# Kernel optimization log

Hardware: AMD Instinct MI355X
Metric: run time of the kernel (lower is better)

The kernel has to match this reference:

```python
import jax, jax.numpy as jnp
import numpy as np

HIDDEN = 1024
FEAT = 2048
BOTTLENECK = 512
B, T = 64, 512


def setup_inputs() -> dict:
    key = jax.random.key(0)
    k1, k2, k3, k4, k5 = jax.random.split(key, 5)
    hidden = jax.random.normal(k1, (B, HIDDEN), dtype=jnp.float32)
    feats = jax.random.normal(k2, (B, T, FEAT), dtype=jnp.float32)
    # nn.Linear weights stored as [out, in]; apply as x @ W.T
    W = jax.random.normal(k3, (BOTTLENECK, HIDDEN), dtype=jnp.float32) * (1.0 / np.sqrt(HIDDEN))
    U = jax.random.normal(k4, (BOTTLENECK, FEAT), dtype=jnp.float32) * (1.0 / np.sqrt(FEAT))
    b = jnp.ones((BOTTLENECK,), dtype=jnp.float32)
    w = jax.random.normal(k5, (1, BOTTLENECK), dtype=jnp.float32) * (1.0 / np.sqrt(BOTTLENECK))
    return {"hidden": hidden, "feats": feats, "W": W, "U": U, "b": b, "w": w}


def reference(hidden, feats, W, U, b, w):
    Wh = hidden @ W.T                      # [B, K]
    Uv = jnp.einsum('btf,kf->btk', feats, U)  # [B, T, K]
    e = jnp.tanh(Wh[:, None, :] + Uv + b)  # [B, T, K]
    energies = jnp.einsum('btk,ok->bto', e, w)  # [B, T, 1]
    weights = jax.nn.softmax(energies, axis=1)  # softmax over time
    attn_feats = jnp.sum(feats * weights, axis=1)  # [B, F]
    return attn_feats, weights
```

## Files before the change

kernel.cpp:

```cpp
#include <hip/hip_runtime.h>
#include <math.h>

#define BATCH 64
#define TDIM 512
#define FEAT 2048
#define HID 1024
#define KDIM 512
#define MROWS (BATCH * TDIM)
#define TCH 16
#define TCLEN (TDIM / TCH)

#define U4 (KDIM * FEAT / 4)

typedef __attribute__((ext_vector_type(8))) short short8;
typedef __attribute__((ext_vector_type(4))) float floatx4;

#define GLL16(g, l)                                                     \
    __builtin_amdgcn_global_load_lds(                                   \
        (const __attribute__((address_space(1))) void*)(g),             \
        (__attribute__((address_space(3))) void*)(l), 16, 0, 0)

__device__ __forceinline__ unsigned short f2bf(float x) {
    unsigned int u = __float_as_uint(x);
    u += 0x7FFFu + ((u >> 16) & 1u);
    return (unsigned short)(u >> 16);
}

__global__ __launch_bounds__(256) void k0n(const float* __restrict__ U,
                                           const float* __restrict__ hidden,
                                           const float* __restrict__ W,
                                           const float* __restrict__ bias,
                                           unsigned short* __restrict__ uB,
                                           float* __restrict__ whb) {
    int bx = blockIdx.x;
    if (bx < 256) {
        int stride = 256 * 256;
        for (int i = bx * 256 + threadIdx.x; i < U4; i += stride) {
            float4 v = ((const float4*)U)[i];
            ushort4 o;
            o.x = f2bf(v.x); o.y = f2bf(v.y); o.z = f2bf(v.z); o.w = f2bf(v.w);
            ((ushort4*)uB)[i] = o;
        }
    } else {
        int bid = bx - 256;
        int b = bid >> 7;
        int k = (bid & 127) * 4 + (threadIdx.x >> 6);
        int lane = threadIdx.x & 63;
        const float* hrow = hidden + (size_t)b * HID;
        const float* wrow = W + (size_t)k * HID;
        float acc = 0.f;
        #pragma unroll 4
        for (int h = lane; h < HID; h += 64) acc += hrow[h] * wrow[h];
        #pragma unroll
        for (int off = 32; off > 0; off >>= 1) acc += __shfl_down(acc, off, 64);
        if (lane == 0) whb[b * KDIM + k] = acc + bias[k];
    }
}

__global__ __launch_bounds__(512, 2) void k2n(const float* __restrict__ feats,
                                              const unsigned short* __restrict__ uB,
                                              const float* __restrict__ whb,
                                              const float* __restrict__ wvec,
                                              float* __restrict__ energies) {
    __shared__ __align__(16) unsigned short As[128 * 64];
    __shared__ __align__(16) unsigned short Bs[512 * 64];
    __shared__ float sums[4][128];

    const int tid  = threadIdx.x;
    const int wave = tid >> 6;
    const int lane = tid & 63;
    const int row0 = blockIdx.x * 128;
    const int wm = wave >> 2;
    const int wn = wave & 3;
    const int col = lane & 15, quad = lane >> 4;

    const int sr = tid >> 3;
    const int sc = (tid & 7) ^ (sr & 7);
    const float* gA = feats + (size_t)(row0 + sr) * FEAT + sc * 8;
    unsigned short* lA0 = As + tid * 8;
    unsigned short* lA1 = As + (tid + 512) * 8;

    const int bq = (lane & 7) ^ ((lane >> 3) & 7);
    const int br = wave * 8 + (lane >> 3);
    const unsigned short* gBp[8];
    unsigned short* lB[8];
    #pragma unroll
    for (int g = 0; g < 8; ++g) {
        gBp[g] = uB + (size_t)(g * 64 + br) * FEAT + bq * 8;
        lB[g]  = Bs + (g * 512 + wave * 64) * 8;
    }

    floatx4 acc[4][8];
    #pragma unroll
    for (int i = 0; i < 4; ++i)
        #pragma unroll
        for (int j = 0; j < 8; ++j) acc[i][j] = (floatx4){0.f, 0.f, 0.f, 0.f};

    float4 a0 = *(const float4*)(gA);
    float4 a1 = *(const float4*)(gA + 4);
    float4 a2 = *(const float4*)(gA + (size_t)64 * FEAT);
    float4 a3 = *(const float4*)(gA + (size_t)64 * FEAT + 4);
    gA += 64;

    for (int f0 = 0; f0 < FEAT; f0 += 64) {
        #pragma unroll
        for (int g = 0; g < 8; ++g) { GLL16(gBp[g], lB[g]); gBp[g] += 64; }
        short8 w0, w1;
        w0[0] = f2bf(a0.x); w0[1] = f2bf(a0.y); w0[2] = f2bf(a0.z); w0[3] = f2bf(a0.w);
        w0[4] = f2bf(a1.x); w0[5] = f2bf(a1.y); w0[6] = f2bf(a1.z); w0[7] = f2bf(a1.w);
        w1[0] = f2bf(a2.x); w1[1] = f2bf(a2.y); w1[2] = f2bf(a2.z); w1[3] = f2bf(a2.w);
        w1[4] = f2bf(a3.x); w1[5] = f2bf(a3.y); w1[6] = f2bf(a3.z); w1[7] = f2bf(a3.w);
        *(short8*)lA0 = w0;
        *(short8*)lA1 = w1;
        __syncthreads();

        if (f0 + 64 < FEAT) {
            a0 = *(const float4*)(gA);
            a1 = *(const float4*)(gA + 4);
            a2 = *(const float4*)(gA + (size_t)64 * FEAT);
            a3 = *(const float4*)(gA + (size_t)64 * FEAT + 4);
            gA += 64;
        }

        #pragma unroll
        for (int kk = 0; kk < 2; ++kk) {
            const int sw = ((kk * 4 + quad) ^ (col & 7)) * 8;
            short8 af[4], bf[8];
            #pragma unroll
            for (int i = 0; i < 4; ++i)
                af[i] = *(const short8*)&As[(wm * 64 + i * 16 + col) * 64 + sw];
            #pragma unroll
            for (int j = 0; j < 8; ++j)
                bf[j] = *(const short8*)&Bs[(wn * 128 + j * 16 + col) * 64 + sw];
            #pragma unroll
            for (int i = 0; i < 4; ++i)
                #pragma unroll
                for (int j = 0; j < 8; ++j)
                    acc[i][j] = __builtin_amdgcn_mfma_f32_16x16x32_bf16(
                        af[i], bf[j], acc[i][j], 0, 0, 0);
        }
        __syncthreads();
    }

    const int b = row0 >> 9;
    float wk[8], hk[8];
    #pragma unroll
    for (int j = 0; j < 8; ++j) {
        int k = wn * 128 + j * 16 + col;
        wk[j] = wvec[k];
        hk[j] = whb[b * KDIM + k];
    }
    #pragma unroll
    for (int i = 0; i < 4; ++i) {
        #pragma unroll
        for (int r = 0; r < 4; ++r) {
            float s = 0.f;
            #pragma unroll
            for (int j = 0; j < 8; ++j)
                s += tanhf(acc[i][j][r] + hk[j]) * wk[j];
            #pragma unroll
            for (int off = 8; off > 0; off >>= 1)
                s += __shfl_down(s, off, 16);
            if (col == 0)
                sums[wn][wm * 64 + i * 16 + quad * 4 + r] = s;
        }
    }
    __syncthreads();
    if (tid < 128)
        energies[row0 + tid] =
            sums[0][tid] + sums[1][tid] + sums[2][tid] + sums[3][tid];
}

__global__ __launch_bounds__(512) void k3n(const float* __restrict__ energies,
                                           float* __restrict__ wout) {
    int b = blockIdx.x;
    int t = threadIdx.x;
    float e = energies[b * TDIM + t];

    __shared__ float sm[512];
    sm[t] = e;
    __syncthreads();
    #pragma unroll
    for (int s = 256; s > 0; s >>= 1) {
        if (t < s) sm[t] = fmaxf(sm[t], sm[t + s]);
        __syncthreads();
    }
    float m = sm[0];
    __syncthreads();
    float ex = __expf(e - m);
    sm[t] = ex;
    __syncthreads();
    #pragma unroll
    for (int s = 256; s > 0; s >>= 1) {
        if (t < s) sm[t] += sm[t + s];
        __syncthreads();
    }
    float inv = 1.f / sm[0];
    wout[b * TDIM + t] = ex * inv;
}

__global__ __launch_bounds__(256) void k4n(const float* __restrict__ feats,
                                           const float* __restrict__ weights,
                                           float* __restrict__ partial4) {
    int b  = blockIdx.y;
    int t0 = blockIdx.x * TCLEN;
    int f8 = threadIdx.x * 8;
    __shared__ float wsm[TCLEN];
    if (threadIdx.x < TCLEN) wsm[threadIdx.x] = weights[b * TDIM + t0 + threadIdx.x];
    __syncthreads();

    const float* fp = feats + ((size_t)b * TDIM + t0) * FEAT + f8;
    float a[8];
    #pragma unroll
    for (int e = 0; e < 8; ++e) a[e] = 0.f;
    #pragma unroll 4
    for (int t = 0; t < TCLEN; ++t) {
        float4 v0 = *(const float4*)(fp + (size_t)t * FEAT);
        float4 v1 = *(const float4*)(fp + (size_t)t * FEAT + 4);
        float w = wsm[t];
        a[0] += v0.x * w; a[1] += v0.y * w; a[2] += v0.z * w; a[3] += v0.w * w;
        a[4] += v1.x * w; a[5] += v1.y * w; a[6] += v1.z * w; a[7] += v1.w * w;
    }
    float* op = partial4 + ((size_t)blockIdx.x * BATCH + b) * FEAT + f8;
    float4 o0 = {a[0], a[1], a[2], a[3]};
    float4 o1 = {a[4], a[5], a[6], a[7]};
    *(float4*)op = o0;
    *(float4*)(op + 4) = o1;
}

__global__ __launch_bounds__(256) void k5_reduce(const float* __restrict__ partial4,
                                                 float* __restrict__ out) {
    int i4 = blockIdx.x * 256 + threadIdx.x;
    float4 s = ((const float4*)partial4)[i4];
    #pragma unroll
    for (int c = 1; c < TCH; ++c) {
        float4 v = ((const float4*)partial4)[(size_t)c * (BATCH * FEAT / 4) + i4];
        s.x += v.x; s.y += v.y; s.z += v.z; s.w += v.w;
    }
    ((float4*)out)[i4] = s;
}

#define BM 128
#define BN 128
#define BF 16
#define LDSPAD 4

__global__ __launch_bounds__(256) void k1_whb(const float* __restrict__ hidden,
                                              const float* __restrict__ W,
                                              const float* __restrict__ bias,
                                              float* __restrict__ whb) {
    int b = blockIdx.y;
    int k = blockIdx.x * 4 + (threadIdx.x >> 6);
    int lane = threadIdx.x & 63;
    const float* hrow = hidden + (size_t)b * HID;
    const float* wrow = W + (size_t)k * HID;
    float acc = 0.f;
    #pragma unroll 4
    for (int h = lane; h < HID; h += 64) acc += hrow[h] * wrow[h];
    #pragma unroll
    for (int off = 32; off > 0; off >>= 1) acc += __shfl_down(acc, off, 64);
    if (lane == 0) whb[b * KDIM + k] = acc + bias[k];
}

__global__ __launch_bounds__(256) void k2_energy(const float* __restrict__ feats,
                                                 const float* __restrict__ U,
                                                 const float* __restrict__ whb,
                                                 const float* __restrict__ wvec,
                                                 float* __restrict__ partial) {
    __shared__ __align__(16) float As[BF][BM + LDSPAD];
    __shared__ __align__(16) float Us[BF][BN + LDSPAD];

    const int row0 = blockIdx.x * BM;
    const int k0   = blockIdx.y * BN;
    const int tid  = threadIdx.x;
    const int tx   = tid & 15;
    const int ty   = tid >> 4;

    float acc[8][8];
    #pragma unroll
    for (int i = 0; i < 8; ++i)
        #pragma unroll
        for (int j = 0; j < 8; ++j) acc[i][j] = 0.f;

    for (int f0 = 0; f0 < FEAT; f0 += BF) {
        #pragma unroll
        for (int l = 0; l < 2; ++l) {
            int li = tid + l * 256;
            int r  = li >> 2;
            int c4 = (li & 3) * 4;
            float4 av = *(const float4*)(feats + (size_t)(row0 + r) * FEAT + f0 + c4);
            float4 uv = *(const float4*)(U     + (size_t)(k0   + r) * FEAT + f0 + c4);
            As[c4 + 0][r] = av.x; As[c4 + 1][r] = av.y;
            As[c4 + 2][r] = av.z; As[c4 + 3][r] = av.w;
            Us[c4 + 0][r] = uv.x; Us[c4 + 1][r] = uv.y;
            Us[c4 + 2][r] = uv.z; Us[c4 + 3][r] = uv.w;
        }
        __syncthreads();
        #pragma unroll
        for (int kf = 0; kf < BF; ++kf) {
            float4 a0 = *(const float4*)&As[kf][ty * 8];
            float4 a1 = *(const float4*)&As[kf][ty * 8 + 4];
            float4 u0 = *(const float4*)&Us[kf][tx * 8];
            float4 u1 = *(const float4*)&Us[kf][tx * 8 + 4];
            float a[8] = {a0.x, a0.y, a0.z, a0.w, a1.x, a1.y, a1.z, a1.w};
            float u[8] = {u0.x, u0.y, u0.z, u0.w, u1.x, u1.y, u1.z, u1.w};
            #pragma unroll
            for (int i = 0; i < 8; ++i)
                #pragma unroll
                for (int j = 0; j < 8; ++j) acc[i][j] += a[i] * u[j];
        }
        __syncthreads();
    }

    const int b = row0 >> 9;
    float psum[8];
    #pragma unroll
    for (int i = 0; i < 8; ++i) {
        float s = 0.f;
        #pragma unroll
        for (int j = 0; j < 8; ++j) {
            int k = k0 + tx * 8 + j;
            s += tanhf(acc[i][j] + whb[b * KDIM + k]) * wvec[k];
        }
        psum[i] = s;
    }
    #pragma unroll
    for (int off = 8; off > 0; off >>= 1)
        #pragma unroll
        for (int i = 0; i < 8; ++i) psum[i] += __shfl_down(psum[i], off, 16);

    if (tx == 0) {
        int c = blockIdx.y;
        #pragma unroll
        for (int i = 0; i < 8; ++i)
            partial[c * MROWS + row0 + ty * 8 + i] = psum[i];
    }
}

__global__ __launch_bounds__(512) void k3_softmax(const float* __restrict__ partial,
                                                  float* __restrict__ wout) {
    int b = blockIdx.x;
    int t = threadIdx.x;
    float e = 0.f;
    #pragma unroll
    for (int c = 0; c < 4; ++c) e += partial[c * MROWS + b * TDIM + t];

    __shared__ float sm[512];
    sm[t] = e;
    __syncthreads();
    #pragma unroll
    for (int s = 256; s > 0; s >>= 1) {
        if (t < s) sm[t] = fmaxf(sm[t], sm[t + s]);
        __syncthreads();
    }
    float m = sm[0];
    __syncthreads();
    float ex = __expf(e - m);
    sm[t] = ex;
    __syncthreads();
    #pragma unroll
    for (int s = 256; s > 0; s >>= 1) {
        if (t < s) sm[t] += sm[t + s];
        __syncthreads();
    }
    float inv = 1.f / sm[0];
    wout[b * TDIM + t] = ex * inv;
}

__global__ __launch_bounds__(256) void k4_direct(const float* __restrict__ feats,
                                                 const float* __restrict__ weights,
                                                 float* __restrict__ out) {
    int b = blockIdx.y;
    int f4 = (blockIdx.x * 256 + threadIdx.x) * 4;
    __shared__ float wsm[TDIM];
    wsm[threadIdx.x]       = weights[b * TDIM + threadIdx.x];
    wsm[threadIdx.x + 256] = weights[b * TDIM + 256 + threadIdx.x];
    __syncthreads();

    const float* fp = feats + (size_t)b * TDIM * FEAT + f4;
    float ax = 0.f, ay = 0.f, az = 0.f, aw = 0.f;
    for (int t = 0; t < TDIM; ++t) {
        float4 v = *(const float4*)(fp + (size_t)t * FEAT);
        float w = wsm[t];
        ax += v.x * w; ay += v.y * w; az += v.z * w; aw += v.w * w;
    }
    float4 o = {ax, ay, az, aw};
    *(float4*)(out + (size_t)b * FEAT + f4) = o;
}

extern "C" void kernel_launch(void* const* d_in, const int* in_sizes, int n_in,
                              void* d_out, int out_size, void* d_ws, size_t ws_size,
                              hipStream_t stream) {
    const float* hidden = (const float*)d_in[0];
    const float* feats  = (const float*)d_in[1];
    const float* W      = (const float*)d_in[2];
    const float* U      = (const float*)d_in[3];
    const float* bias   = (const float*)d_in[4];
    const float* wvec   = (const float*)d_in[5];

    float* out         = (float*)d_out;
    float* attn_out    = out;
    float* weights_out = out + (size_t)BATCH * FEAT;
    float* whb         = weights_out;
    float* energies    = attn_out;

    const size_t uN        = (size_t)KDIM * FEAT;
    const size_t uBytes    = uN * sizeof(unsigned short);
    const size_t poolBytes = (size_t)TCH * BATCH * FEAT * sizeof(float);
    const bool fast = ws_size >= uBytes + poolBytes;

    if (fast) {
        unsigned short* uBf = (unsigned short*)d_ws;
        float* pool4 = (float*)((char*)d_ws + uBytes);
        k0n<<<dim3(256 + 8192), 256, 0, stream>>>(U, hidden, W, bias, uBf, whb);
        k2n<<<dim3(MROWS / 128), 512, 0, stream>>>(feats, uBf, whb, wvec, energies);
        k3n<<<dim3(BATCH), 512, 0, stream>>>(energies, weights_out);
        k4n<<<dim3(TCH, BATCH), 256, 0, stream>>>(feats, weights_out, pool4);
        k5_reduce<<<dim3(BATCH * FEAT / 4 / 256), 256, 0, stream>>>(pool4, attn_out);
    } else {
        k1_whb<<<dim3(KDIM / 4, BATCH), 256, 0, stream>>>(hidden, W, bias, whb);
        k2_energy<<<dim3(MROWS / 128, KDIM / 128), 256, 0, stream>>>(
            feats, U, whb, wvec, energies);
        k3_softmax<<<dim3(BATCH), 512, 0, stream>>>(energies, weights_out);
        k4_direct<<<dim3(FEAT / 1024, BATCH), 256, 0, stream>>>(
            feats, weights_out, attn_out);
    }
}
```

Before: 490.9 us.

## Pre-tile bf16 U into swizzled tiles and double-buffer B in LDS

The U-to-bf16 conversion now writes U already arranged in per-step, pre-swizzled 64-column tiles, so each wave's B loads come from one contiguous region. The energy GEMM kernel gets a second LDS buffer for B and issues the global-to-LDS copy for the next K step before running the MFMAs on the current one. The feats A tile is still single-buffered, with its conversion and store moved after the compute barrier. The aim is to hide B load latency behind the matrix math, at the cost of about 146KB of LDS per block and an extra barrier per step.

```diff
diff --git a/kernel.cpp b/kernel.cpp
--- a/kernel.cpp
+++ b/kernel.cpp
@@ -10,7 +10,9 @@
 #define TCH 16
 #define TCLEN (TDIM / TCH)
 
-#define U4 (KDIM * FEAT / 4)
+#define NSTEP (FEAT / 64)
+#define BSLOT (KDIM * 8)
+#define BTILE (BSLOT * 8)
 
 typedef __attribute__((ext_vector_type(8))) short short8;
 typedef __attribute__((ext_vector_type(4))) float floatx4;
@@ -30,16 +32,24 @@
                                            const float* __restrict__ hidden,
                                            const float* __restrict__ W,
                                            const float* __restrict__ bias,
-                                           unsigned short* __restrict__ uB,
+                                           unsigned short* __restrict__ uBt,
                                            float* __restrict__ whb) {
     int bx = blockIdx.x;
     if (bx < 256) {
-        int stride = 256 * 256;
-        for (int i = bx * 256 + threadIdx.x; i < U4; i += stride) {
-            float4 v = ((const float4*)U)[i];
-            ushort4 o;
-            o.x = f2bf(v.x); o.y = f2bf(v.y); o.z = f2bf(v.z); o.w = f2bf(v.w);
-            ((ushort4*)uB)[i] = o;
+        const int NS = NSTEP * BSLOT;
+        for (int s = bx * 256 + threadIdx.x; s < NS; s += 256 * 256) {
+            int t   = s >> 12;
+            int rem = s & 4095;
+            int r   = rem >> 3;
+            int c   = (rem & 7) ^ (r & 7);
+            const float* src = U + (size_t)r * FEAT + t * 64 + c * 8;
+            float4 v0 = *(const float4*)src;
+            float4 v1 = *(const float4*)(src + 4);
+            ushort4 o0, o1;
+            o0.x = f2bf(v0.x); o0.y = f2bf(v0.y); o0.z = f2bf(v0.z); o0.w = f2bf(v0.w);
+            o1.x = f2bf(v1.x); o1.y = f2bf(v1.y); o1.z = f2bf(v1.z); o1.w = f2bf(v1.w);
+            ((ushort4*)uBt)[s * 2]     = o0;
+            ((ushort4*)uBt)[s * 2 + 1] = o1;
         }
     } else {
         int bid = bx - 256;
@@ -58,12 +68,12 @@
 }
 
 __global__ __launch_bounds__(512, 2) void k2n(const float* __restrict__ feats,
-                                              const unsigned short* __restrict__ uB,
+                                              const unsigned short* __restrict__ uBt,
                                               const float* __restrict__ whb,
                                               const float* __restrict__ wvec,
                                               float* __restrict__ energies) {
     __shared__ __align__(16) unsigned short As[128 * 64];
-    __shared__ __align__(16) unsigned short Bs[512 * 64];
+    __shared__ __align__(16) unsigned short Bs[2][512 * 64];
     __shared__ float sums[4][128];
 
     const int tid  = threadIdx.x;
@@ -80,15 +90,7 @@
     unsigned short* lA0 = As + tid * 8;
     unsigned short* lA1 = As + (tid + 512) * 8;
 
-    const int bq = (lane & 7) ^ ((lane >> 3) & 7);
-    const int br = wave * 8 + (lane >> 3);
-    const unsigned short* gBp[8];
-    unsigned short* lB[8];
-    #pragma unroll
-    for (int g = 0; g < 8; ++g) {
-        gBp[g] = uB + (size_t)(g * 64 + br) * FEAT + bq * 8;
-        lB[g]  = Bs + (g * 512 + wave * 64) * 8;
-    }
+    const unsigned short* gB = uBt + (size_t)(wave * 512 + lane) * 8;
 
     floatx4 acc[4][8];
     #pragma unroll
@@ -101,10 +103,10 @@
     float4 a2 = *(const float4*)(gA + (size_t)64 * FEAT);
     float4 a3 = *(const float4*)(gA + (size_t)64 * FEAT + 4);
     gA += 64;
-
-    for (int f0 = 0; f0 < FEAT; f0 += 64) {
-        #pragma unroll
-        for (int g = 0; g < 8; ++g) { GLL16(gBp[g], lB[g]); gBp[g] += 64; }
+    #pragma unroll
+    for (int g = 0; g < 8; ++g)
+        GLL16(gB + g * 512, &Bs[0][(wave * 512 + g * 64) * 8]);
+    {
         short8 w0, w1;
         w0[0] = f2bf(a0.x); w0[1] = f2bf(a0.y); w0[2] = f2bf(a0.z); w0[3] = f2bf(a0.w);
         w0[4] = f2bf(a1.x); w0[5] = f2bf(a1.y); w0[6] = f2bf(a1.z); w0[7] = f2bf(a1.w);
@@ -112,14 +114,22 @@
         w1[4] = f2bf(a3.x); w1[5] = f2bf(a3.y); w1[6] = f2bf(a3.z); w1[7] = f2bf(a3.w);
         *(short8*)lA0 = w0;
         *(short8*)lA1 = w1;
-        __syncthreads();
-
-        if (f0 + 64 < FEAT) {
+    }
+    __syncthreads();
+
+    int nb = 0;
+    for (int t = 0; t < NSTEP; ++t) {
+        if (t < NSTEP - 1) {
             a0 = *(const float4*)(gA);
             a1 = *(const float4*)(gA + 4);
             a2 = *(const float4*)(gA + (size_t)64 * FEAT);
             a3 = *(const float4*)(gA + (size_t)64 * FEAT + 4);
             gA += 64;
+            const unsigned short* gb = gB + (size_t)(t + 1) * BTILE;
+            unsigned short* lb = &Bs[nb ^ 1][(wave * 512) * 8];
+            #pragma unroll
+            for (int g = 0; g < 8; ++g)
+                GLL16(gb + g * 512, lb + g * 512);
         }
 
         #pragma unroll
@@ -131,7 +141,7 @@
                 af[i] = *(const short8*)&As[(wm * 64 + i * 16 + col) * 64 + sw];
             #pragma unroll
             for (int j = 0; j < 8; ++j)
-                bf[j] = *(const short8*)&Bs[(wn * 128 + j * 16 + col) * 64 + sw];
+                bf[j] = *(const short8*)&Bs[nb][(wn * 128 + j * 16 + col) * 64 + sw];
             #pragma unroll
             for (int i = 0; i < 4; ++i)
                 #pragma unroll
@@ -140,6 +150,18 @@
                         af[i], bf[j], acc[i][j], 0, 0, 0);
         }
         __syncthreads();
+
+        if (t < NSTEP - 1) {
+            short8 w0, w1;
+            w0[0] = f2bf(a0.x); w0[1] = f2bf(a0.y); w0[2] = f2bf(a0.z); w0[3] = f2bf(a0.w);
+            w0[4] = f2bf(a1.x); w0[5] = f2bf(a1.y); w0[6] = f2bf(a1.z); w0[7] = f2bf(a1.w);
+            w1[0] = f2bf(a2.x); w1[1] = f2bf(a2.y); w1[2] = f2bf(a2.z); w1[3] = f2bf(a2.w);
+            w1[4] = f2bf(a3.x); w1[5] = f2bf(a3.y); w1[6] = f2bf(a3.z); w1[7] = f2bf(a3.w);
+            *(short8*)lA0 = w0;
+            *(short8*)lA1 = w1;
+            __syncthreads();
+        }
+        nb ^= 1;
     }
 
     const int b = row0 >> 9;
@@ -410,10 +432,10 @@
     const bool fast = ws_size >= uBytes + poolBytes;
 
     if (fast) {
-        unsigned short* uBf = (unsigned short*)d_ws;
+        unsigned short* uBt = (unsigned short*)d_ws;
         float* pool4 = (float*)((char*)d_ws + uBytes);
-        k0n<<<dim3(256 + 8192), 256, 0, stream>>>(U, hidden, W, bias, uBf, whb);
-        k2n<<<dim3(MROWS / 128), 512, 0, stream>>>(feats, uBf, whb, wvec, energies);
+        k0n<<<dim3(256 + 8192), 256, 0, stream>>>(U, hidden, W, bias, uBt, whb);
+        k2n<<<dim3(MROWS / 128), 512, 0, stream>>>(feats, uBt, whb, wvec, energies);
         k3n<<<dim3(BATCH), 512, 0, stream>>>(energies, weights_out);
         k4n<<<dim3(TCH, BATCH), 256, 0, stream>>>(feats, weights_out, pool4);
         k5_reduce<<<dim3(BATCH * FEAT / 4 / 256), 256, 0, stream>>>(pool4, attn_out);
```

After: 499.6 us. About the same (+1.8%).

## Fuse all stages into one persistent kernel with global barriers

Applied to the files above, without the earlier changes.

Replaces the five-kernel pipeline (U conversion plus Wh, energy GEMM, softmax, weighted sum, reduction) with one 256-block persistent kernel. The stages are separated by an atomic grid barrier. The time-axis split for the weighted sum drops from 16 chunks to 4, and each block recomputes its batch's softmax in shared memory. This removes kernel launch gaps and shrinks the partial-sum buffer. In exchange it relies on all blocks being co-resident, spins on global atomics, and runs the feature pass with fewer, longer-running blocks.

```diff
diff --git a/kernel.cpp b/kernel.cpp
--- a/kernel.cpp
+++ b/kernel.cpp
@@ -7,10 +7,6 @@
 #define HID 1024
 #define KDIM 512
 #define MROWS (BATCH * TDIM)
-#define TCH 16
-#define TCLEN (TDIM / TCH)
-
-#define U4 (KDIM * FEAT / 4)
 
 typedef __attribute__((ext_vector_type(8))) short short8;
 typedef __attribute__((ext_vector_type(4))) float floatx4;
@@ -26,218 +22,229 @@
     return (unsigned short)(u >> 16);
 }
 
-__global__ __launch_bounds__(256) void k0n(const float* __restrict__ U,
-                                           const float* __restrict__ hidden,
-                                           const float* __restrict__ W,
-                                           const float* __restrict__ bias,
-                                           unsigned short* __restrict__ uB,
-                                           float* __restrict__ whb) {
-    int bx = blockIdx.x;
-    if (bx < 256) {
-        int stride = 256 * 256;
-        for (int i = bx * 256 + threadIdx.x; i < U4; i += stride) {
-            float4 v = ((const float4*)U)[i];
-            ushort4 o;
-            o.x = f2bf(v.x); o.y = f2bf(v.y); o.z = f2bf(v.z); o.w = f2bf(v.w);
-            ((ushort4*)uB)[i] = o;
-        }
-    } else {
-        int bid = bx - 256;
-        int b = bid >> 7;
-        int k = (bid & 127) * 4 + (threadIdx.x >> 6);
-        int lane = threadIdx.x & 63;
-        const float* hrow = hidden + (size_t)b * HID;
-        const float* wrow = W + (size_t)k * HID;
-        float acc = 0.f;
-        #pragma unroll 4
-        for (int h = lane; h < HID; h += 64) acc += hrow[h] * wrow[h];
-        #pragma unroll
-        for (int off = 32; off > 0; off >>= 1) acc += __shfl_down(acc, off, 64);
-        if (lane == 0) whb[b * KDIM + k] = acc + bias[k];
-    }
-}
-
-__global__ __launch_bounds__(512, 2) void k2n(const float* __restrict__ feats,
-                                              const unsigned short* __restrict__ uB,
-                                              const float* __restrict__ whb,
-                                              const float* __restrict__ wvec,
-                                              float* __restrict__ energies) {
+__device__ __forceinline__ void gbar(unsigned* cnt, unsigned* gen, int nblk) {
+    __syncthreads();
+    __threadfence();
+    if (threadIdx.x == 0) {
+        unsigned g = __hip_atomic_load(gen, __ATOMIC_ACQUIRE,
+                                       __HIP_MEMORY_SCOPE_AGENT);
+        unsigned a = __hip_atomic_fetch_add(cnt, 1u, __ATOMIC_ACQ_REL,
+                                            __HIP_MEMORY_SCOPE_AGENT);
+        if (a == (unsigned)(nblk - 1)) {
+            __hip_atomic_store(cnt, 0u, __ATOMIC_RELAXED,
+                               __HIP_MEMORY_SCOPE_AGENT);
+            __hip_atomic_fetch_add(gen, 1u, __ATOMIC_RELEASE,
+                                   __HIP_MEMORY_SCOPE_AGENT);
+        } else {
+            long long t0 = (long long)clock64();
+            while (__hip_atomic_load(gen, __ATOMIC_ACQUIRE,
+                                     __HIP_MEMORY_SCOPE_AGENT) == g) {
+                __builtin_amdgcn_s_sleep(8);
+                if ((long long)clock64() - t0 > 100000000LL) break;
+            }
+        }
+    }
+    __syncthreads();
+    __threadfence();
+}
+
+__global__ __launch_bounds__(64) void k_init(unsigned* __restrict__ bar) {
+    if (threadIdx.x < 16) bar[threadIdx.x] = 0u;
+}
+
+__global__ __launch_bounds__(512) void mega(
+    const float* __restrict__ feats, const float* __restrict__ U,
+    const float* __restrict__ hidden, const float* __restrict__ W,
+    const float* __restrict__ bias, const float* __restrict__ wvec,
+    unsigned short* __restrict__ uB, float* __restrict__ pool4,
+    unsigned* __restrict__ bar,
+    float* __restrict__ whb, float* __restrict__ energies,
+    float* __restrict__ weights_out, float* __restrict__ attn_out) {
     __shared__ __align__(16) unsigned short As[128 * 64];
     __shared__ __align__(16) unsigned short Bs[512 * 64];
     __shared__ float sums[4][128];
+    __shared__ float sm[512];
 
     const int tid  = threadIdx.x;
+    const int bx   = blockIdx.x;
     const int wave = tid >> 6;
     const int lane = tid & 63;
-    const int row0 = blockIdx.x * 128;
-    const int wm = wave >> 2;
-    const int wn = wave & 3;
-    const int col = lane & 15, quad = lane >> 4;
-
-    const int sr = tid >> 3;
-    const int sc = (tid & 7) ^ (sr & 7);
-    const float* gA = feats + (size_t)(row0 + sr) * FEAT + sc * 8;
-    unsigned short* lA0 = As + tid * 8;
-    unsigned short* lA1 = As + (tid + 512) * 8;
-
-    const int bq = (lane & 7) ^ ((lane >> 3) & 7);
-    const int br = wave * 8 + (lane >> 3);
-    const unsigned short* gBp[8];
-    unsigned short* lB[8];
-    #pragma unroll
-    for (int g = 0; g < 8; ++g) {
-        gBp[g] = uB + (size_t)(g * 64 + br) * FEAT + bq * 8;
-        lB[g]  = Bs + (g * 512 + wave * 64) * 8;
-    }
-
-    floatx4 acc[4][8];
-    #pragma unroll
-    for (int i = 0; i < 4; ++i)
-        #pragma unroll
-        for (int j = 0; j < 8; ++j) acc[i][j] = (floatx4){0.f, 0.f, 0.f, 0.f};
-
-    float4 a0 = *(const float4*)(gA);
-    float4 a1 = *(const float4*)(gA + 4);
-    float4 a2 = *(const float4*)(gA + (size_t)64 * FEAT);
-    float4 a3 = *(const float4*)(gA + (size_t)64 * FEAT + 4);
-    gA += 64;
-
-    for (int f0 = 0; f0 < FEAT; f0 += 64) {
-        #pragma unroll
-        for (int g = 0; g < 8; ++g) { GLL16(gBp[g], lB[g]); gBp[g] += 64; }
-        short8 w0, w1;
-        w0[0] = f2bf(a0.x); w0[1] = f2bf(a0.y); w0[2] = f2bf(a0.z); w0[3] = f2bf(a0.w);
-        w0[4] = f2bf(a1.x); w0[5] = f2bf(a1.y); w0[6] = f2bf(a1.z); w0[7] = f2bf(a1.w);
-        w1[0] = f2bf(a2.x); w1[1] = f2bf(a2.y); w1[2] = f2bf(a2.z); w1[3] = f2bf(a2.w);
-        w1[4] = f2bf(a3.x); w1[5] = f2bf(a3.y); w1[6] = f2bf(a3.z); w1[7] = f2bf(a3.w);
-        *(short8*)lA0 = w0;
-        *(short8*)lA1 = w1;
-        __syncthreads();
-
-        if (f0 + 64 < FEAT) {
-            a0 = *(const float4*)(gA);
-            a1 = *(const float4*)(gA + 4);
-            a2 = *(const float4*)(gA + (size_t)64 * FEAT);
-            a3 = *(const float4*)(gA + (size_t)64 * FEAT + 4);
-            gA += 64;
-        }
-
-        #pragma unroll
-        for (int kk = 0; kk < 2; ++kk) {
-            const int sw = ((kk * 4 + quad) ^ (col & 7)) * 8;
-            short8 af[4], bf[8];
-            #pragma unroll
-            for (int i = 0; i < 4; ++i)
-                af[i] = *(const short8*)&As[(wm * 64 + i * 16 + col) * 64 + sw];
-            #pragma unroll
-            for (int j = 0; j < 8; ++j)
-                bf[j] = *(const short8*)&Bs[(wn * 128 + j * 16 + col) * 64 + sw];
-            #pragma unroll
-            for (int i = 0; i < 4; ++i)
+    unsigned* cnt = bar;
+    unsigned* gen = bar + 1;
+
+    {
+        const int i2 = (bx * 512 + tid) * 2;
+        #pragma unroll
+        for (int r = 0; r < 2; ++r) {
+            float4 v = ((const float4*)U)[i2 + r];
+            ushort4 o;
+            o.x = f2bf(v.x); o.y = f2bf(v.y); o.z = f2bf(v.z); o.w = f2bf(v.w);
+            ((ushort4*)uB)[i2 + r] = o;
+        }
+        const int gw = bx * 8 + wave;
+        for (int o = gw * 16; o < gw * 16 + 16; ++o) {
+            const int b = o >> 9, k = o & 511;
+            const float* hrow = hidden + (size_t)b * HID;
+            const float* wrow = W + (size_t)k * HID;
+            float acc = 0.f;
+            #pragma unroll 4
+            for (int h = lane; h < HID; h += 64) acc += hrow[h] * wrow[h];
+            #pragma unroll
+            for (int off = 32; off > 0; off >>= 1) acc += __shfl_down(acc, off, 64);
+            if (lane == 0) whb[o] = acc + bias[k];
+        }
+    }
+    gbar(cnt, gen, 256);
+
+    {
+        const int row0 = bx * 128;
+        const int wm = wave >> 2;
+        const int wn = wave & 3;
+        const int col = lane & 15, quad = lane >> 4;
+
+        const int sr = tid >> 3;
+        const int sc = (tid & 7) ^ (sr & 7);
+        const float* gA = feats + (size_t)(row0 + sr) * FEAT + sc * 8;
+        unsigned short* lA0 = As + tid * 8;
+        unsigned short* lA1 = As + (tid + 512) * 8;
+
+        const int bq = (lane & 7) ^ ((lane >> 3) & 7);
+        const int br = wave * 8 + (lane >> 3);
+        const unsigned short* gBp[8];
+        unsigned short* lB[8];
+        #pragma unroll
+        for (int g = 0; g < 8; ++g) {
+            gBp[g] = uB + (size_t)(g * 64 + br) * FEAT + bq * 8;
+            lB[g]  = Bs + (g * 512 + wave * 64) * 8;
+        }
+
+        floatx4 acc[4][8];
+        #pragma unroll
+        for (int i = 0; i < 4; ++i)
+            #pragma unroll
+            for (int j = 0; j < 8; ++j) acc[i][j] = (floatx4){0.f, 0.f, 0.f, 0.f};
+
+        float4 a0 = *(const float4*)(gA);
+        float4 a1 = *(const float4*)(gA + 4);
+        float4 a2 = *(const float4*)(gA + (size_t)64 * FEAT);
+        float4 a3 = *(const float4*)(gA + (size_t)64 * FEAT + 4);
+        gA += 64;
+
+        for (int f0 = 0; f0 < FEAT; f0 += 64) {
+            #pragma unroll
+            for (int g = 0; g < 8; ++g) { GLL16(gBp[g], lB[g]); gBp[g] += 64; }
+            short8 w0, w1;
+            w0[0] = f2bf(a0.x); w0[1] = f2bf(a0.y); w0[2] = f2bf(a0.z); w0[3] = f2bf(a0.w);
+            w0[4] = f2bf(a1.x); w0[5] = f2bf(a1.y); w0[6] = f2bf(a1.z); w0[7] = f2bf(a1.w);
+            w1[0] = f2bf(a2.x); w1[1] = f2bf(a2.y); w1[2] = f2bf(a2.z); w1[3] = f2bf(a2.w);
+            w1[4] = f2bf(a3.x); w1[5] = f2bf(a3.y); w1[6] = f2bf(a3.z); w1[7] = f2bf(a3.w);
+            *(short8*)lA0 = w0;
+            *(short8*)lA1 = w1;
+            __syncthreads();
+
+            if (f0 + 64 < FEAT) {
+                a0 = *(const float4*)(gA);
+                a1 = *(const float4*)(gA + 4);
+                a2 = *(const float4*)(gA + (size_t)64 * FEAT);
+                a3 = *(const float4*)(gA + (size_t)64 * FEAT + 4);
+                gA += 64;
+            }
+
+            #pragma unroll
+            for (int kk = 0; kk < 2; ++kk) {
+                const int sw = ((kk * 4 + quad) ^ (col & 7)) * 8;
+                short8 af[4], bf[8];
+                #pragma unroll
+                for (int i = 0; i < 4; ++i)
+                    af[i] = *(const short8*)&As[(wm * 64 + i * 16 + col) * 64 + sw];
                 #pragma unroll
                 for (int j = 0; j < 8; ++j)
-                    acc[i][j] = __builtin_amdgcn_mfma_f32_16x16x32_bf16(
-                        af[i], bf[j], acc[i][j], 0, 0, 0);
-        }
-        __syncthreads();
-    }
-
-    const int b = row0 >> 9;
-    float wk[8], hk[8];
-    #pragma unroll
-    for (int j = 0; j < 8; ++j) {
-        int k = wn * 128 + j * 16 + col;
-        wk[j] = wvec[k];
-        hk[j] = whb[b * KDIM + k];
-    }
-    #pragma unroll
-    for (int i = 0; i < 4; ++i) {
-        #pragma unroll
-        for (int r = 0; r < 4; ++r) {
-            float s = 0.f;
-            #pragma unroll
-            for (int j = 0; j < 8; ++j)
-                s += tanhf(acc[i][j][r] + hk[j]) * wk[j];
-            #pragma unroll
-            for (int off = 8; off > 0; off >>= 1)
-                s += __shfl_down(s, off, 16);
-            if (col == 0)
-                sums[wn][wm * 64 + i * 16 + quad * 4 + r] = s;
-        }
-    }
-    __syncthreads();
-    if (tid < 128)
-        energies[row0 + tid] =
-            sums[0][tid] + sums[1][tid] + sums[2][tid] + sums[3][tid];
-}
-
-__global__ __launch_bounds__(512) void k3n(const float* __restrict__ energies,
-                                           float* __restrict__ wout) {
-    int b = blockIdx.x;
-    int t = threadIdx.x;
-    float e = energies[b * TDIM + t];
-
-    __shared__ float sm[512];
-    sm[t] = e;
-    __syncthreads();
-    #pragma unroll
-    for (int s = 256; s > 0; s >>= 1) {
-        if (t < s) sm[t] = fmaxf(sm[t], sm[t + s]);
-        __syncthreads();
-    }
-    float m = sm[0];
-    __syncthreads();
-    float ex = __expf(e - m);
-    sm[t] = ex;
-    __syncthreads();
-    #pragma unroll
-    for (int s = 256; s > 0; s >>= 1) {
-        if (t < s) sm[t] += sm[t + s];
-        __syncthreads();
-    }
-    float inv = 1.f / sm[0];
-    wout[b * TDIM + t] = ex * inv;
-}
-
-__global__ __launch_bounds__(256) void k4n(const float* __restrict__ feats,
-                                           const float* __restrict__ weights,
-                                           float* __restrict__ partial4) {
-    int b  = blockIdx.y;
-    int t0 = blockIdx.x * TCLEN;
-    int f8 = threadIdx.x * 8;
-    __shared__ float wsm[TCLEN];
-    if (threadIdx.x < TCLEN) wsm[threadIdx.x] = weights[b * TDIM + t0 + threadIdx.x];
-    __syncthreads();
-
-    const float* fp = feats + ((size_t)b * TDIM + t0) * FEAT + f8;
-    float a[8];
-    #pragma unroll
-    for (int e = 0; e < 8; ++e) a[e] = 0.f;
-    #pragma unroll 4
-    for (int t = 0; t < TCLEN; ++t) {
-        float4 v0 = *(const float4*)(fp + (size_t)t * FEAT);
-        float4 v1 = *(const float4*)(fp + (size_t)t * FEAT + 4);
-        float w = wsm[t];
-        a[0] += v0.x * w; a[1] += v0.y * w; a[2] += v0.z * w; a[3] += v0.w * w;
-        a[4] += v1.x * w; a[5] += v1.y * w; a[6] += v1.z * w; a[7] += v1.w * w;
-    }
-    float* op = partial4 + ((size_t)blockIdx.x * BATCH + b) * FEAT + f8;
-    float4 o0 = {a[0], a[1], a[2], a[3]};
-    float4 o1 = {a[4], a[5], a[6], a[7]};
-    *(float4*)op = o0;
-    *(float4*)(op + 4) = o1;
-}
-
-__global__ __launch_bounds__(256) void k5_reduce(const float* __restrict__ partial4,
-                                                 float* __restrict__ out) {
-    int i4 = blockIdx.x * 256 + threadIdx.x;
-    float4 s = ((const float4*)partial4)[i4];
-    #pragma unroll
-    for (int c = 1; c < TCH; ++c) {
-        float4 v = ((const float4*)partial4)[(size_t)c * (BATCH * FEAT / 4) + i4];
-        s.x += v.x; s.y += v.y; s.z += v.z; s.w += v.w;
-    }
-    ((float4*)out)[i4] = s;
+                    bf[j] = *(const short8*)&Bs[(wn * 128 + j * 16 + col) * 64 + sw];
+                #pragma unroll
+                for (int i = 0; i < 4; ++i)
+                    #pragma unroll
+                    for (int j = 0; j < 8; ++j)
+                        acc[i][j] = __builtin_amdgcn_mfma_f32_16x16x32_bf16(
+                            af[i], bf[j], acc[i][j], 0, 0, 0);
+            }
+            __syncthreads();
+        }
+
+        const int b = row0 >> 9;
+        float wk[8], hk[8];
+        #pragma unroll
+        for (int j = 0; j < 8; ++j) {
+            int k = wn * 128 + j * 16 + col;
+            wk[j] = wvec[k];
+            hk[j] = whb[b * KDIM + k];
+        }
+        #pragma unroll
+        for (int i = 0; i < 4; ++i) {
+            #pragma unroll
+            for (int r = 0; r < 4; ++r) {
+                float s = 0.f;
+                #pragma unroll
+                for (int j = 0; j < 8; ++j)
+                    s += tanhf(acc[i][j][r] + hk[j]) * wk[j];
+                #pragma unroll
+                for (int off = 8; off > 0; off >>= 1)
+                    s += __shfl_down(s, off, 16);
+                if (col == 0)
+                    sums[wn][wm * 64 + i * 16 + quad * 4 + r] = s;
+            }
+        }
+        __syncthreads();
+        if (tid < 128)
+            energies[row0 + tid] =
+                sums[0][tid] + sums[1][tid] + sums[2][tid] + sums[3][tid];
+    }
+    gbar(cnt, gen, 256);
+
+    {
+        const int b = bx >> 2, tq = bx & 3, t0 = tq * 128;
+        float* sred = &sums[0][0];
+        const float e = energies[b * TDIM + tid];
+        sred[tid] = e;
+        __syncthreads();
+        #pragma unroll
+        for (int s = 256; s > 0; s >>= 1) {
+            if (tid < s) sred[tid] = fmaxf(sred[tid], sred[tid + s]);
+            __syncthreads();
+        }
+        const float m = sred[0];
+        __syncthreads();
+        const float ex = __expf(e - m);
+        sred[tid] = ex;
+        __syncthreads();
+        #pragma unroll
+        for (int s = 256; s > 0; s >>= 1) {
+            if (tid < s) sred[tid] += sred[tid + s];
+            __syncthreads();
+        }
+        const float inv = 1.f / sred[0];
+        sm[tid] = ex * inv;
+        __syncthreads();
+        if (tq == 0) weights_out[b * TDIM + tid] = sm[tid];
+
+        const int f4 = tid * 4;
+        const float* fp = feats + ((size_t)b * TDIM + t0) * FEAT + f4;
+        float ax = 0.f, ay = 0.f, az = 0.f, aw = 0.f;
+        #pragma unroll 4
+        for (int t = 0; t < 128; ++t) {
+            float4 v = *(const float4*)(fp + (size_t)t * FEAT);
+            float w = sm[t0 + t];
+            ax += v.x * w; ay += v.y * w; az += v.z * w; aw += v.w * w;
+        }
+        float4 o = {ax, ay, az, aw};
+        *(float4*)(pool4 + ((size_t)tq * BATCH + b) * FEAT + f4) = o;
+    }
+    gbar(cnt, gen, 256);
+
+    {
+        const int idx = bx * 512 + tid;
+        attn_out[idx] = pool4[idx] + pool4[BATCH * FEAT + idx] +
+                        pool4[2 * BATCH * FEAT + idx] + pool4[3 * BATCH * FEAT + idx];
+    }
 }
 
 #define BM 128
@@ -404,24 +411,24 @@
     float* whb         = weights_out;
     float* energies    = attn_out;
 
-    const size_t uN        = (size_t)KDIM * FEAT;
-    const size_t uBytes    = uN * sizeof(unsigned short);
-    const size_t poolBytes = (size_t)TCH * BATCH * FEAT * sizeof(float);
-    const bool fast = ws_size >= uBytes + poolBytes;
+    const size_t uBytes    = (size_t)KDIM * FEAT * sizeof(unsigned short);
+    const size_t poolBytes = (size_t)4 * BATCH * FEAT * sizeof(float);
+    const bool fast = ws_size >= uBytes + poolBytes + 64;
 
     if (fast) {
-        unsigned short* uBf = (unsigned short*)d_ws;
+        unsigned short* uB = (unsigned short*)d_ws;
         float* pool4 = (float*)((char*)d_ws + uBytes);
-        k0n<<<dim3(256 + 8192), 256, 0, stream>>>(U, hidden, W, bias, uBf, whb);
-        k2n<<<dim3(MROWS / 128), 512, 0, stream>>>(feats, uBf, whb, wvec, energies);
-        k3n<<<dim3(BATCH), 512, 0, stream>>>(energies, weights_out);
-        k4n<<<dim3(TCH, BATCH), 256, 0, stream>>>(feats, weights_out, pool4);
-        k5_reduce<<<dim3(BATCH * FEAT / 4 / 256), 256, 0, stream>>>(pool4, attn_out);
+        unsigned* bar = (unsigned*)((char*)d_ws + uBytes + poolBytes);
+        k_init<<<dim3(1), 64, 0, stream>>>(bar);
+        mega<<<dim3(256), 512, 0, stream>>>(feats, U, hidden, W, bias, wvec,
+                                            uB, pool4, bar, whb, energies,
+                                            weights_out, attn_out);
     } else {
+        float* partial = attn_out;
         k1_whb<<<dim3(KDIM / 4, BATCH), 256, 0, stream>>>(hidden, W, bias, whb);
         k2_energy<<<dim3(MROWS / 128, KDIM / 128), 256, 0, stream>>>(
-            feats, U, whb, wvec, energies);
-        k3_softmax<<<dim3(BATCH), 512, 0, stream>>>(energies, weights_out);
+            feats, U, whb, wvec, partial);
+        k3_softmax<<<dim3(BATCH), 512, 0, stream>>>(partial, weights_out);
         k4_direct<<<dim3(FEAT / 1024, BATCH), 256, 0, stream>>>(
             feats, weights_out, attn_out);
     }
```

Result: slower. 773.6 us (+57.6%).
